# Optimization experiments

Measured on AMD Instinct MI355X. Metric: run time of the kernel, lower is better.

## Reference

```python
import jax, jax.numpy as jnp
import numpy as np

TOKEN_BITS = 10
CODEBOOK_SIZE = 2 ** TOKEN_BITS  # 1024
COMMITMENT_COST = 0.25
ENTROPY_LOSS_WEIGHT = 0.1
ENTROPY_TEMPERATURE = 0.01
ENTROPY_GAMMA = 1.0
EPS = 1e-5


def _make_codebook():
    bits_to_indices = (2 ** jnp.arange(TOKEN_BITS)).astype(jnp.int32)          # [c]
    all_codes = jnp.arange(CODEBOOK_SIZE, dtype=jnp.int32)                      # [n]
    bits = ((all_codes[:, None] & bits_to_indices) != 0).astype(jnp.float32)    # [n, c]
    codebook = bits * 2.0 - 1.0                                                 # [n, c] in {-1,+1}
    return bits_to_indices, codebook


def setup_inputs() -> dict:
    key = jax.random.key(0)
    z = jax.random.normal(key, (16, TOKEN_BITS, 64, 64), dtype=jnp.float32)
    return {"z": z}


def reference(z):
    bits_to_indices, codebook = _make_codebook()

    # b c h w -> b h w c
    zp = jnp.transpose(z, (0, 2, 3, 1)).astype(jnp.float32)

    # sign quantization to {-1, +1}
    sign_mask = zp > 0.0
    z_q = jnp.where(sign_mask, 1.0, -1.0).astype(jnp.float32)

    # pack sign bits into codebook indices
    min_encoding_indices = jnp.sum(sign_mask.astype(jnp.int32) * bits_to_indices, axis=-1)  # [b,h,w]

    # commitment loss (stop-grad on the quantized target)
    commitment_loss = COMMITMENT_COST * jnp.mean((jax.lax.stop_gradient(z_q) - zp) ** 2)

    # entropy loss: logits = -d = 2 * z . codebook^T, softened by temperature
    logits = 2.0 * jnp.einsum('bhwc,nc->bhwn', zp, codebook)  # [b,h,w,n]
    log_probs = jax.nn.log_softmax(logits / ENTROPY_TEMPERATURE, axis=-1)
    probs = jnp.exp(log_probs)
    per_sample_entropy = jnp.mean(-jnp.sum(probs * log_probs, axis=-1))
    avg_probs = jnp.mean(probs, axis=(0, 1, 2))  # [n]
    avg_entropy = ENTROPY_GAMMA * (-jnp.sum(avg_probs * jnp.log(avg_probs + EPS)))
    entropy_loss = ENTROPY_LOSS_WEIGHT * (per_sample_entropy - avg_entropy)

    loss = commitment_loss + entropy_loss

    # straight-through estimator
    z_quantized = zp + jax.lax.stop_gradient(z_q - zp)
    # b h w c -> b c h w
    z_quantized = jnp.transpose(z_quantized, (0, 3, 1, 2))

    return z_quantized, loss, per_sample_entropy, min_encoding_indices
```

## Files before the change

kernel.cpp:

```cpp
#include <hip/hip_runtime.h>

#define NCH    10
#define NCODE  1024
#define NLOC   65536
#define NZ     655360
#define GRID   1024
#define THR    128
#define LPB    64
#define NHIST  8
#define NPART  (GRID * 2)

__device__ __forceinline__ float wave_reduce_sum(float v) {
#pragma unroll
    for (int off = 32; off > 0; off >>= 1)
        v += __shfl_down(v, off, 64);
    return v;
}

__global__ __launch_bounds__(THR) void lfq_main(
    const float* __restrict__ z, float* __restrict__ out,
    float* __restrict__ wsH, float* __restrict__ wsC, float* __restrict__ wsE)
{
    const int tid  = threadIdx.x;
    const int wv   = tid >> 6;
    const int lane = tid & 63;
    const int sub  = lane >> 5;
    const int l32  = lane & 31;
    const int lloc = wv * 32 + l32;
    const int loc  = blockIdx.x * LPB + lloc;
    const int b    = loc >> 12;
    const int base = b * (NCH * 4096) + (loc & 4095);
    const int c0   = sub * 5;
    float* hist = wsH + (blockIdx.x & (NHIST - 1)) * NCODE;

    float zc[5];
#pragma unroll
    for (int i = 0; i < 5; ++i)
        zc[i] = z[base + (c0 + i) * 4096];

    float commit = 0.f, ent = 0.f, pstar = 1.f;
    float r[5];
    int idx = 0;
#pragma unroll
    for (int i = 0; i < 5; ++i) {
        float zv = zc[i];
        bool bit = zv > 0.f;
        float s = bit ? 1.f : -1.f;
        out[base + (c0 + i) * 4096] = s;
        if (bit) idx |= (1 << (c0 + i));
        float d = s - zv;
        commit += d * d;
        float a = fabsf(zv) * 400.f;
        float e = __expf(-a);
        float inv = 1.f / (1.f + e);
        ent += __logf(1.f + e) + a * e * inv;
        pstar *= inv;
        r[i] = (a < 23.0f) ? e : 0.f;
    }

    const int   idx_o = __shfl_xor(idx, 32, 64);
    const float p_o   = __shfl_xor(pstar, 32, 64);
    float ro[5];
#pragma unroll
    for (int i = 0; i < 5; ++i) ro[i] = __shfl_xor(r[i], 32, 64);

    float cw = wave_reduce_sum(commit);
    float ew = wave_reduce_sum(ent);
    if (lane == 0) {
        wsC[blockIdx.x * 2 + wv] = cw;
        wsE[blockIdx.x * 2 + wv] = ew;
    }

    const int idxT = idx | idx_o;
    const float pT = pstar * p_o;
    const float rr0 = sub ? ro[0] : r[0], rr1 = sub ? ro[1] : r[1],
                rr2 = sub ? ro[2] : r[2], rr3 = sub ? ro[3] : r[3],
                rr4 = sub ? ro[4] : r[4];
    const float rr5 = sub ? r[0] : ro[0], rr6 = sub ? r[1] : ro[1],
                rr7 = sub ? r[2] : ro[2], rr8 = sub ? r[3] : ro[3],
                rr9 = sub ? r[4] : ro[4];
    const unsigned M =
          (rr0 > 0.f ? 1u : 0u)   | (rr1 > 0.f ? 2u : 0u)
        | (rr2 > 0.f ? 4u : 0u)   | (rr3 > 0.f ? 8u : 0u)
        | (rr4 > 0.f ? 16u : 0u)  | (rr5 > 0.f ? 32u : 0u)
        | (rr6 > 0.f ? 64u : 0u)  | (rr7 > 0.f ? 128u : 0u)
        | (rr8 > 0.f ? 256u : 0u) | (rr9 > 0.f ? 512u : 0u);
    const unsigned L  = M & (unsigned)(-(int)M);
    const unsigned Mp = M ^ L;

    auto wsub = [&](unsigned s) {
        float w = pT;
        if (s & 1u)   w *= rr0;
        if (s & 2u)   w *= rr1;
        if (s & 4u)   w *= rr2;
        if (s & 8u)   w *= rr3;
        if (s & 16u)  w *= rr4;
        if (s & 32u)  w *= rr5;
        if (s & 64u)  w *= rr6;
        if (s & 128u) w *= rr7;
        if (s & 256u) w *= rr8;
        if (s & 512u) w *= rr9;
        return w;
    };

    if (sub == 0) {
        atomicAdd(&hist[idxT], pT);
        if (L) {
            unsigned t = Mp;
            for (;;) {
                const unsigned s = t | L;
                atomicAdd(&hist[idxT ^ (int)s], wsub(s));
                if (!t) break;
                t = (t - 1) & Mp;
            }
        }
    } else {
        out[NZ + 2 + loc] = (float)idxT;
        unsigned t = Mp;
        while (t) {
            atomicAdd(&hist[idxT ^ (int)t], wsub(t));
            t = (t - 1) & Mp;
        }
    }
}

__global__ __launch_bounds__(1024) void lfq_final(
    const float* __restrict__ wsH, const float* __restrict__ wsC,
    const float* __restrict__ wsE, float* __restrict__ out)
{
    const int n = threadIdx.x;
    float s = 0.f;
#pragma unroll
    for (int h = 0; h < NHIST; ++h) s += wsH[h * NCODE + n];
    float avg_p = s * (1.f / (float)NLOC);
    float term = -avg_p * __logf(avg_p + 1e-5f);
    float c = wsC[n] + wsC[1024 + n];
    float e = wsE[n] + wsE[1024 + n];
    float tw = wave_reduce_sum(term);
    float cw = wave_reduce_sum(c);
    float ew = wave_reduce_sum(e);
    __shared__ float red[48];
    const int wave = n >> 6, lane = n & 63;
    if (lane == 0) { red[wave] = tw; red[16 + wave] = cw; red[32 + wave] = ew; }
    __syncthreads();
    if (n == 0) {
        float avg_ent = 0.f, cs = 0.f, es = 0.f;
#pragma unroll
        for (int w = 0; w < 16; ++w) {
            avg_ent += red[w]; cs += red[16 + w]; es += red[32 + w];
        }
        float commitment = 0.25f * cs * (1.f / (float)NZ);
        float per_sample = es * (1.f / (float)NLOC);
        out[NZ]     = commitment + 0.1f * (per_sample - avg_ent);
        out[NZ + 1] = per_sample;
    }
}

extern "C" void kernel_launch(void* const* d_in, const int* in_sizes, int n_in,
                              void* d_out, int out_size, void* d_ws, size_t ws_size,
                              hipStream_t stream) {
    const float* z = (const float*)d_in[0];
    float* out = (float*)d_out;
    float* wsH = (float*)d_ws;
    float* wsC = wsH + NHIST * NCODE;
    float* wsE = wsC + NPART;

    lfq_main<<<GRID, THR, 0, stream>>>(z, out, wsH, wsC, wsE);
    lfq_final<<<1, 1024, 0, stream>>>(wsH, wsC, wsE, out);
}
```

Before: 63.98 us.

## Fuse final reduction into main kernel via last-block completion counter

Merges the two kernels into one. Every block increments a global counter, and the last block to finish reduces the histograms and loss partials to write the scalar outputs. Commit and entropy partials are now accumulated with atomics into 128 slots, and the launch shape changes to 512 blocks of 256 threads. This removes a kernel launch and the gap between the two kernels, in exchange for extra atomics, a fence, and a serial tail in one block. It also relies on the workspace being zeroed before each call, and the counter check includes an odd special case for a poisoned value.

```diff
diff --git a/kernel.cpp b/kernel.cpp
--- a/kernel.cpp
+++ b/kernel.cpp
@@ -4,11 +4,13 @@
 #define NCODE  1024
 #define NLOC   65536
 #define NZ     655360
-#define GRID   1024
-#define THR    128
-#define LPB    64
+#define GRID   512
+#define THR    256
+#define LPB    128
 #define NHIST  8
-#define NPART  (GRID * 2)
+#define WS_C   (NHIST * NCODE)
+#define WS_E   (WS_C + 128)
+#define WS_CNT (WS_E + 128)
 
 __device__ __forceinline__ float wave_reduce_sum(float v) {
 #pragma unroll
@@ -17,10 +19,13 @@
     return v;
 }
 
-__global__ __launch_bounds__(THR) void lfq_main(
+__global__ __launch_bounds__(THR) void lfq_fused(
     const float* __restrict__ z, float* __restrict__ out,
-    float* __restrict__ wsH, float* __restrict__ wsC, float* __restrict__ wsE)
+    float* __restrict__ ws)
 {
+    __shared__ unsigned s_last;
+    __shared__ float red[12];
+
     const int tid  = threadIdx.x;
     const int wv   = tid >> 6;
     const int lane = tid & 63;
@@ -31,7 +36,7 @@
     const int b    = loc >> 12;
     const int base = b * (NCH * 4096) + (loc & 4095);
     const int c0   = sub * 5;
-    float* hist = wsH + (blockIdx.x & (NHIST - 1)) * NCODE;
+    float* hist = ws + (blockIdx.x & (NHIST - 1)) * NCODE;
 
     float zc[5];
 #pragma unroll
@@ -67,8 +72,8 @@
     float cw = wave_reduce_sum(commit);
     float ew = wave_reduce_sum(ent);
     if (lane == 0) {
-        wsC[blockIdx.x * 2 + wv] = cw;
-        wsE[blockIdx.x * 2 + wv] = ew;
+        atomicAdd(&ws[WS_C + (blockIdx.x & 127)], cw);
+        atomicAdd(&ws[WS_E + (blockIdx.x & 127)], ew);
     }
 
     const int idxT = idx | idx_o;
@@ -122,37 +127,48 @@
             t = (t - 1) & Mp;
         }
     }
-}
 
-__global__ __launch_bounds__(1024) void lfq_final(
-    const float* __restrict__ wsH, const float* __restrict__ wsC,
-    const float* __restrict__ wsE, float* __restrict__ out)
-{
-    const int n = threadIdx.x;
-    float s = 0.f;
+    __syncthreads();
+    if (tid == 0) {
+        __threadfence();
+        unsigned old = atomicAdd((unsigned*)(ws + WS_CNT), 1u);
+        unsigned rem = old + 1u - (unsigned)GRID;
+        s_last = (rem == 0u || rem == 0xAAAAAAAAu) ? 1u : 0u;
+    }
+    __syncthreads();
+    if (s_last) {
+        __threadfence();
+        float tpart = 0.f;
+        for (int n = tid; n < NCODE; n += THR) {
+            float s = 0.f;
 #pragma unroll
-    for (int h = 0; h < NHIST; ++h) s += wsH[h * NCODE + n];
-    float avg_p = s * (1.f / (float)NLOC);
-    float term = -avg_p * __logf(avg_p + 1e-5f);
-    float c = wsC[n] + wsC[1024 + n];
-    float e = wsE[n] + wsE[1024 + n];
-    float tw = wave_reduce_sum(term);
-    float cw = wave_reduce_sum(c);
-    float ew = wave_reduce_sum(e);
-    __shared__ float red[48];
-    const int wave = n >> 6, lane = n & 63;
-    if (lane == 0) { red[wave] = tw; red[16 + wave] = cw; red[32 + wave] = ew; }
-    __syncthreads();
-    if (n == 0) {
-        float avg_ent = 0.f, cs = 0.f, es = 0.f;
-#pragma unroll
-        for (int w = 0; w < 16; ++w) {
-            avg_ent += red[w]; cs += red[16 + w]; es += red[32 + w];
+            for (int h = 0; h < NHIST; ++h)
+                s += __hip_atomic_load(&ws[h * NCODE + n],
+                        __ATOMIC_RELAXED, __HIP_MEMORY_SCOPE_AGENT);
+            float avg_p = s * (1.f / (float)NLOC);
+            tpart += -avg_p * __logf(avg_p + 1e-5f);
         }
-        float commitment = 0.25f * cs * (1.f / (float)NZ);
-        float per_sample = es * (1.f / (float)NLOC);
-        out[NZ]     = commitment + 0.1f * (per_sample - avg_ent);
-        out[NZ + 1] = per_sample;
+        float cpart = 0.f, epart = 0.f;
+        if (tid < 128) {
+            cpart = __hip_atomic_load(&ws[WS_C + tid],
+                        __ATOMIC_RELAXED, __HIP_MEMORY_SCOPE_AGENT);
+            epart = __hip_atomic_load(&ws[WS_E + tid],
+                        __ATOMIC_RELAXED, __HIP_MEMORY_SCOPE_AGENT);
+        }
+        float tw  = wave_reduce_sum(tpart);
+        float cw2 = wave_reduce_sum(cpart);
+        float ew2 = wave_reduce_sum(epart);
+        if (lane == 0) { red[wv] = tw; red[4 + wv] = cw2; red[8 + wv] = ew2; }
+        __syncthreads();
+        if (tid == 0) {
+            float avg_ent = red[0] + red[1] + red[2] + red[3];
+            float cs = red[4] + red[5] + red[6] + red[7];
+            float es = red[8] + red[9] + red[10] + red[11];
+            float commitment = 0.25f * cs * (1.f / (float)NZ);
+            float per_sample = es * (1.f / (float)NLOC);
+            out[NZ]     = commitment + 0.1f * (per_sample - avg_ent);
+            out[NZ + 1] = per_sample;
+        }
     }
 }
 
@@ -161,10 +177,6 @@
                               hipStream_t stream) {
     const float* z = (const float*)d_in[0];
     float* out = (float*)d_out;
-    float* wsH = (float*)d_ws;
-    float* wsC = wsH + NHIST * NCODE;
-    float* wsE = wsC + NPART;
-
-    lfq_main<<<GRID, THR, 0, stream>>>(z, out, wsH, wsC, wsE);
-    lfq_final<<<1, 1024, 0, stream>>>(wsH, wsC, wsE, out);
+    float* ws  = (float*)d_ws;
+    lfq_fused<<<GRID, THR, 0, stream>>>(z, out, ws);
 }
```

Result: slower. 76.24 us (+19.2%).
